# Optimization experiments

Hardware: AMD Instinct MI355X
Metric: run time of the kernel (lower is better)

## Reference

```python
import jax, jax.numpy as jnp
import numpy as np

V = 196608   # HEALPix nside=128 pixels
NNZ = 9 * V  # ~8 neighbors + self loop per pixel
B, FIN, FOUT, K = 4, 32, 64, 5


def setup_inputs() -> dict:
    key = jax.random.key(0)
    k1, k2, k3, k4, k5, k6 = jax.random.split(key, 6)
    lap_rows = jax.random.randint(k1, (NNZ,), 0, V, dtype=jnp.int32)
    lap_cols = jax.random.randint(k2, (NNZ,), 0, V, dtype=jnp.int32)
    # scale values so the Chebyshev recurrence stays numerically tame
    lap_vals = jax.random.normal(k3, (NNZ,), dtype=jnp.float32) * 0.1
    inputs = jax.random.normal(k4, (B, V, FIN), dtype=jnp.float32)
    std = np.sqrt(2.0 / (FIN + FOUT)).astype(np.float32)  # xavier normal
    weight = jax.random.normal(k5, (K, FIN, FOUT), dtype=jnp.float32) * std
    bias = jnp.full((FOUT,), 0.01, dtype=jnp.float32)
    return {"lap_rows": lap_rows, "lap_cols": lap_cols, "lap_vals": lap_vals,
            "inputs": inputs, "weight": weight, "bias": bias}


def reference(lap_rows, lap_cols, lap_vals, inputs, weight, bias):
    Bq, Vq, Fin = inputs.shape
    Kq, _, Fout = weight.shape

    # x0: [V, Fin*B]  (matches torch permute(1,2,0).reshape)
    x0 = jnp.transpose(inputs, (1, 2, 0)).reshape(Vq, Fin * Bq)

    def spmm(x):  # sparse [V,V] @ dense [V, Fin*B] via gather + scatter-add
        contrib = lap_vals[:, None] * x[lap_cols]  # [nnz, Fin*B]
        return jax.ops.segment_sum(contrib, lap_rows, num_segments=Vq)

    xs = [x0]
    if Kq > 1:
        xs.append(spmm(x0))
    for _ in range(2, Kq):
        xs.append(2.0 * spmm(xs[-1]) - xs[-2])
    cheb = jnp.stack(xs)  # [K, V, Fin*B]

    # [K,V,Fin,B] -> [B,V,Fin,K] -> [B*V, Fin*K]
    cheb = cheb.reshape(Kq, Vq, Fin, Bq).transpose(3, 1, 2, 0).reshape(Bq * Vq, Fin * Kq)
    # torch weight.view(Fin*K, Fout) flattens (K,Fin) row-major -> reshape(K*Fin, Fout)
    w2 = weight.reshape(Kq * Fin, Fout)
    out = (cheb @ w2).reshape(Bq, Vq, Fout)
    return out + bias
```

## Files before the change

### kernel.cpp

```cpp
#include <hip/hip_runtime.h>

#define V 196608
#define NNZ (9 * V)
#define B 4
#define FIN 32
#define FOUT 64
#define K 5
#define C 128
#define ROWU 64
#define SPMM_BLOCKS 2048
#define NSLICE 864
#define EDGES_PER_SLICE 2048
#define HIST_BLOCKS (NNZ / 256)
#define X0_BLOCKS (V * 16 / 256)
#define WFRAG_BLOCKS 5

typedef __attribute__((ext_vector_type(8))) short bf16x8;
typedef __attribute__((ext_vector_type(4))) float f32x4;

static __device__ __forceinline__ unsigned int f2bf(float f) {
    union { float f; unsigned int u; } v; v.f = f;
    return (v.u + 0x7FFFu + ((v.u >> 16) & 1u)) >> 16;
}
static __device__ __forceinline__ float bflo(unsigned int u) {
    union { unsigned int u; float f; } v; v.u = u << 16; return v.f;
}
static __device__ __forceinline__ float bfhi(unsigned int u) {
    union { unsigned int u; float f; } v; v.u = u & 0xFFFF0000u; return v.f;
}

__global__ void zero_cursor(uint4* __restrict__ p) {
    int t = blockIdx.x * 256 + threadIdx.x;
    if (t < V / 4) p[t] = (uint4){0u, 0u, 0u, 0u};
}

__global__ void prep_fused(const int* __restrict__ rows, int* __restrict__ cnt,
                           int* __restrict__ rank, const float* __restrict__ inp,
                           uint4* __restrict__ x0v, const float* __restrict__ w,
                           uint4* __restrict__ wfh, uint4* __restrict__ wfl) {
    const int blk = blockIdx.x;
    if (blk < HIST_BLOCKS) {
        int e = blk * 256 + threadIdx.x;
        rank[e] = atomicAdd(&cnt[rows[e]], 1);
    } else if (blk < HIST_BLOCKS + X0_BLOCKS) {
        int t = (blk - HIST_BLOCKS) * 256 + threadIdx.x;
        int v = t >> 4;
        int seg = t & 15;
        int b = seg >> 2;
        int q = seg & 3;
        const float4* s =
            reinterpret_cast<const float4*>(inp + ((size_t)b * V + v) * 32 + q * 8);
        float4 fa = s[0], fb = s[1];
        uint4 u;
        u.x = f2bf(fa.x) | (f2bf(fa.y) << 16);
        u.y = f2bf(fa.z) | (f2bf(fa.w) << 16);
        u.z = f2bf(fb.x) | (f2bf(fb.y) << 16);
        u.w = f2bf(fb.z) | (f2bf(fb.w) << 16);
        x0v[(size_t)v * 16 + seg] = u;
    } else {
        int idx = (blk - HIST_BLOCKS - X0_BLOCKS) * 256 + threadIdx.x;
        if (idx >= K * 4 * 64) return;
        int lane = idx & 63;
        int nt = (idx >> 6) & 3;
        int k = idx >> 8;
        int col = lane & 15;
        int quad = lane >> 4;
        int o = nt * 16 + col;
        unsigned int hh[8], ll[8];
#pragma unroll
        for (int e = 0; e < 8; ++e) {
            int fin = quad * 8 + e;
            float wv = w[(fin * 5 + k) * 64 + o];
            unsigned int hb = f2bf(wv);
            float hf = bflo(hb);
            ll[e] = f2bf(wv - hf);
            hh[e] = hb;
        }
        uint4 uh, ul;
        uh.x = hh[0] | (hh[1] << 16);
        uh.y = hh[2] | (hh[3] << 16);
        uh.z = hh[4] | (hh[5] << 16);
        uh.w = hh[6] | (hh[7] << 16);
        ul.x = ll[0] | (ll[1] << 16);
        ul.y = ll[2] | (ll[3] << 16);
        ul.z = ll[4] | (ll[5] << 16);
        ul.w = ll[6] | (ll[7] << 16);
        wfh[idx] = uh;
        wfl[idx] = ul;
    }
}

__global__ void chunk_sums(const int* __restrict__ cnt, int* __restrict__ bsum) {
    __shared__ int ws[16];
    int tid = threadIdx.x;
    int lane = tid & 63;
    int wid = tid >> 6;
    int v = cnt[blockIdx.x * 1024 + tid];
#pragma unroll
    for (int off = 32; off >= 1; off >>= 1) v += __shfl_down(v, off, 64);
    if (lane == 0) ws[wid] = v;
    __syncthreads();
    if (tid < 16) {
        int s = ws[tid];
#pragma unroll
        for (int off = 8; off >= 1; off >>= 1) s += __shfl_down(s, off, 16);
        if (tid == 0) bsum[blockIdx.x] = s;
    }
}

__global__ void scan_chunks2(const int* __restrict__ cnt, const int* __restrict__ bsum,
                             int* __restrict__ rowptr) {
    __shared__ int sb[192];
    __shared__ int wsum[16];
    int tid = threadIdx.x;
    int lane = tid & 63;
    int wid = tid >> 6;
    if (tid < 192) sb[tid] = bsum[tid];
    __syncthreads();
    for (int off = 1; off < 192; off <<= 1) {
        int v = (tid < 192 && tid >= off) ? sb[tid - off] : 0;
        __syncthreads();
        if (tid < 192) sb[tid] += v;
        __syncthreads();
    }
    const int bpre = (blockIdx.x == 0) ? 0 : sb[blockIdx.x - 1];
    int base = blockIdx.x * 1024;
    int v = cnt[base + tid];
    int x = v;
#pragma unroll
    for (int off = 1; off < 64; off <<= 1) {
        int t = __shfl_up(x, off, 64);
        if (lane >= off) x += t;
    }
    if (lane == 63) wsum[wid] = x;
    __syncthreads();
    if (wid == 0 && lane < 16) {
        int s = wsum[lane];
        int y = s;
#pragma unroll
        for (int off = 1; off < 16; off <<= 1) {
            int t = __shfl_up(y, off, 16);
            if (lane >= off) y += t;
        }
        wsum[lane] = y - s;
    }
    __syncthreads();
    int excl = x - v + wsum[wid] + bpre;
    rowptr[base + tid] = excl;
    if (blockIdx.x == 191 && tid == 1023) rowptr[V] = excl + v;
}

__global__ void scatter_rank(const int* __restrict__ rows, const int* __restrict__ cols,
                             const float* __restrict__ vals, const int* __restrict__ rowptr,
                             const int* __restrict__ rank, int2* __restrict__ cev) {
    const int slice = blockIdx.x >> 3;
    const int w = blockIdx.x & 7;
    const int lo = w * (NNZ / 8);
    const int hi = lo + (NNZ / 8);
    const int base = slice * EDGES_PER_SLICE;
#pragma unroll 2
    for (int i = threadIdx.x; i < EDGES_PER_SLICE; i += 256) {
        int e = base + i;
        int p = rowptr[rows[e]] + rank[e];
        if (p >= lo && p < hi) {
            int2 pk;
            pk.x = cols[e];
            pk.y = __float_as_int(vals[e]);
            cev[p] = pk;
        }
    }
}

template <int COMBINE>
__global__ __launch_bounds__(256) void spmm_gather(
    const int* __restrict__ rowptr, const int2* __restrict__ cev,
    const unsigned int* __restrict__ x, const unsigned int* __restrict__ xm2,
    unsigned int* __restrict__ y) {
    const int lane = threadIdx.x & 63;
    const int wid0 = (blockIdx.x * 256 + threadIdx.x) >> 6;
    const int NW = SPMM_BLOCKS * 4;
    for (int base = wid0 * 2; base < V; base += NW * 2) {
        const int r0 = base, r1 = base + 1;
        const int s0 = rowptr[r0];
        const int e0 = rowptr[r0 + 1];
        const int e1 = rowptr[r1 + 1];
        float ax0 = 0.f, ay0 = 0.f, ax1 = 0.f, ay1 = 0.f;
        int i0 = s0, i1 = e0;
        while (e0 - i0 >= 4 && e1 - i1 >= 4) {
            int2 Ea[4], Eb[4];
#pragma unroll
            for (int j = 0; j < 4; ++j) {
                Ea[j] = cev[i0 + j];
                Eb[j] = cev[i1 + j];
            }
            unsigned int Ua[4], Ub[4];
#pragma unroll
            for (int j = 0; j < 4; ++j) {
                Ua[j] = x[(size_t)Ea[j].x * ROWU + lane];
                Ub[j] = x[(size_t)Eb[j].x * ROWU + lane];
            }
#pragma unroll
            for (int j = 0; j < 4; ++j) {
                float va = __int_as_float(Ea[j].y);
                float vb = __int_as_float(Eb[j].y);
                ax0 = fmaf(va, bflo(Ua[j]), ax0);
                ay0 = fmaf(va, bfhi(Ua[j]), ay0);
                ax1 = fmaf(vb, bflo(Ub[j]), ax1);
                ay1 = fmaf(vb, bfhi(Ub[j]), ay1);
            }
            i0 += 4;
            i1 += 4;
        }
        while (e0 - i0 >= 4) {
            int2 Ea[4];
#pragma unroll
            for (int j = 0; j < 4; ++j) Ea[j] = cev[i0 + j];
            unsigned int Ua[4];
#pragma unroll
            for (int j = 0; j < 4; ++j) Ua[j] = x[(size_t)Ea[j].x * ROWU + lane];
#pragma unroll
            for (int j = 0; j < 4; ++j) {
                float va = __int_as_float(Ea[j].y);
                ax0 = fmaf(va, bflo(Ua[j]), ax0);
                ay0 = fmaf(va, bfhi(Ua[j]), ay0);
            }
            i0 += 4;
        }
        while (e1 - i1 >= 4) {
            int2 Eb[4];
#pragma unroll
            for (int j = 0; j < 4; ++j) Eb[j] = cev[i1 + j];
            unsigned int Ub[4];
#pragma unroll
            for (int j = 0; j < 4; ++j) Ub[j] = x[(size_t)Eb[j].x * ROWU + lane];
#pragma unroll
            for (int j = 0; j < 4; ++j) {
                float vb = __int_as_float(Eb[j].y);
                ax1 = fmaf(vb, bflo(Ub[j]), ax1);
                ay1 = fmaf(vb, bfhi(Ub[j]), ay1);
            }
            i1 += 4;
        }
        for (; i0 + 2 <= e0; i0 += 2) {
            int2 a = cev[i0], b = cev[i0 + 1];
            unsigned int u0 = x[(size_t)a.x * ROWU + lane];
            unsigned int u1 = x[(size_t)b.x * ROWU + lane];
            float v0 = __int_as_float(a.y), v1 = __int_as_float(b.y);
            ax0 = fmaf(v0, bflo(u0), ax0);
            ay0 = fmaf(v0, bfhi(u0), ay0);
            ax0 = fmaf(v1, bflo(u1), ax0);
            ay0 = fmaf(v1, bfhi(u1), ay0);
        }
        for (; i0 < e0; ++i0) {
            int2 a = cev[i0];
            unsigned int u = x[(size_t)a.x * ROWU + lane];
            float v = __int_as_float(a.y);
            ax0 = fmaf(v, bflo(u), ax0);
            ay0 = fmaf(v, bfhi(u), ay0);
        }
        for (; i1 + 2 <= e1; i1 += 2) {
            int2 a = cev[i1], b = cev[i1 + 1];
            unsigned int u0 = x[(size_t)a.x * ROWU + lane];
            unsigned int u1 = x[(size_t)b.x * ROWU + lane];
            float v0 = __int_as_float(a.y), v1 = __int_as_float(b.y);
            ax1 = fmaf(v0, bflo(u0), ax1);
            ay1 = fmaf(v0, bfhi(u0), ay1);
            ax1 = fmaf(v1, bflo(u1), ax1);
            ay1 = fmaf(v1, bfhi(u1), ay1);
        }
        for (; i1 < e1; ++i1) {
            int2 a = cev[i1];
            unsigned int u = x[(size_t)a.x * ROWU + lane];
            float v = __int_as_float(a.y);
            ax1 = fmaf(v, bflo(u), ax1);
            ay1 = fmaf(v, bfhi(u), ay1);
        }
        if (COMBINE) {
            unsigned int m0 = xm2[(size_t)r0 * ROWU + lane];
            unsigned int m1 = xm2[(size_t)r1 * ROWU + lane];
            ax0 = 2.0f * ax0 - bflo(m0);
            ay0 = 2.0f * ay0 - bfhi(m0);
            ax1 = 2.0f * ax1 - bflo(m1);
            ay1 = 2.0f * ay1 - bfhi(m1);
        }
        y[(size_t)r0 * ROWU + lane] = f2bf(ax0) | (f2bf(ay0) << 16);
        y[(size_t)r1 * ROWU + lane] = f2bf(ax1) | (f2bf(ay1) << 16);
    }
}

__global__ __launch_bounds__(256) void fused_mfma(
    const unsigned short* __restrict__ x0, const unsigned short* __restrict__ x1,
    const unsigned short* __restrict__ x2, const unsigned short* __restrict__ x3,
    const unsigned short* __restrict__ x4, const uint4* __restrict__ wfh,
    const uint4* __restrict__ wfl, const float* __restrict__ bias,
    float* __restrict__ out) {
    const int tid = threadIdx.x;
    const int lane = tid & 63;
    const int g = (blockIdx.x * 256 + tid) >> 6;
    const int v0 = g << 4;
    const int col = lane & 15;
    const int quad = lane >> 4;
    const unsigned short* const xs[K] = {x0, x1, x2, x3, x4};

    f32x4 acc[B][4];
#pragma unroll
    for (int b = 0; b < B; ++b)
#pragma unroll
        for (int nt = 0; nt < 4; ++nt) acc[b][nt] = (f32x4){0.f, 0.f, 0.f, 0.f};

#pragma unroll
    for (int k = 0; k < K; ++k) {
        const unsigned short* xk = xs[k] + ((size_t)(v0 + col)) * C + quad * 8;
        bf16x8 a0 = *reinterpret_cast<const bf16x8*>(xk);
        bf16x8 a1 = *reinterpret_cast<const bf16x8*>(xk + 32);
        bf16x8 a2 = *reinterpret_cast<const bf16x8*>(xk + 64);
        bf16x8 a3 = *reinterpret_cast<const bf16x8*>(xk + 96);
#pragma unroll
        for (int nt = 0; nt < 4; ++nt) {
            uint4 uh = wfh[(k * 4 + nt) * 64 + lane];
            uint4 ul = wfl[(k * 4 + nt) * 64 + lane];
            bf16x8 wh = *reinterpret_cast<bf16x8*>(&uh);
            bf16x8 wl = *reinterpret_cast<bf16x8*>(&ul);
            acc[0][nt] = __builtin_amdgcn_mfma_f32_16x16x32_bf16(a0, wh, acc[0][nt], 0, 0, 0);
            acc[1][nt] = __builtin_amdgcn_mfma_f32_16x16x32_bf16(a1, wh, acc[1][nt], 0, 0, 0);
            acc[2][nt] = __builtin_amdgcn_mfma_f32_16x16x32_bf16(a2, wh, acc[2][nt], 0, 0, 0);
            acc[3][nt] = __builtin_amdgcn_mfma_f32_16x16x32_bf16(a3, wh, acc[3][nt], 0, 0, 0);
            acc[0][nt] = __builtin_amdgcn_mfma_f32_16x16x32_bf16(a0, wl, acc[0][nt], 0, 0, 0);
            acc[1][nt] = __builtin_amdgcn_mfma_f32_16x16x32_bf16(a1, wl, acc[1][nt], 0, 0, 0);
            acc[2][nt] = __builtin_amdgcn_mfma_f32_16x16x32_bf16(a2, wl, acc[2][nt], 0, 0, 0);
            acc[3][nt] = __builtin_amdgcn_mfma_f32_16x16x32_bf16(a3, wl, acc[3][nt], 0, 0, 0);
        }
    }

    float bv[4];
#pragma unroll
    for (int nt = 0; nt < 4; ++nt) bv[nt] = bias[nt * 16 + col];
#pragma unroll
    for (int b = 0; b < B; ++b)
#pragma unroll
        for (int nt = 0; nt < 4; ++nt)
#pragma unroll
            for (int r = 0; r < 4; ++r) {
                int row = quad * 4 + r;
                out[((size_t)b * V + v0 + row) * FOUT + nt * 16 + col] = acc[b][nt][r] + bv[nt];
            }
}

extern "C" void kernel_launch(void* const* d_in, const int* in_sizes, int n_in,
                              void* d_out, int out_size, void* d_ws, size_t ws_size,
                              hipStream_t stream) {
    const int* lap_rows = (const int*)d_in[0];
    const int* lap_cols = (const int*)d_in[1];
    const float* lap_vals = (const float*)d_in[2];
    const float* inputs = (const float*)d_in[3];
    const float* weight = (const float*)d_in[4];
    const float* bias = (const float*)d_in[5];
    float* out = (float*)d_out;

    char* p = (char*)d_ws;
    auto alloc = [&](size_t bytes) {
        char* r = p;
        p += (bytes + 511) & ~(size_t)511;
        return r;
    };
    int* rowptr = (int*)alloc((size_t)(V + 1) * 4);
    int* cnt = (int*)alloc((size_t)V * 4);
    int* bsum = (int*)alloc(192 * 4);
    int* rank = (int*)alloc((size_t)NNZ * 4);
    uint4* wfh = (uint4*)alloc((size_t)K * 4 * 64 * 16);
    uint4* wfl = (uint4*)alloc((size_t)K * 4 * 64 * 16);
    int2* cev = (int2*)alloc((size_t)NNZ * 8);
    unsigned int* xb0 = (unsigned int*)alloc((size_t)V * ROWU * 4);
    unsigned int* xb1 = (unsigned int*)alloc((size_t)V * ROWU * 4);
    unsigned int* xb2 = (unsigned int*)alloc((size_t)V * ROWU * 4);
    unsigned int* xb3 = (unsigned int*)alloc((size_t)V * ROWU * 4);
    unsigned int* xb4 = (unsigned int*)alloc((size_t)V * ROWU * 4);

    const int mfma_blocks = (V / 16) * 64 / 256;
    const int prep_blocks = HIST_BLOCKS + X0_BLOCKS + WFRAG_BLOCKS;

    zero_cursor<<<(V / 4 + 255) / 256, 256, 0, stream>>>((uint4*)cnt);
    prep_fused<<<prep_blocks, 256, 0, stream>>>(lap_rows, cnt, rank, inputs, (uint4*)xb0,
                                                weight, wfh, wfl);
    chunk_sums<<<V / 1024, 1024, 0, stream>>>(cnt, bsum);
    scan_chunks2<<<V / 1024, 1024, 0, stream>>>(cnt, bsum, rowptr);
    scatter_rank<<<NSLICE * 8, 256, 0, stream>>>(lap_rows, lap_cols, lap_vals, rowptr,
                                                 rank, cev);

    spmm_gather<0><<<SPMM_BLOCKS, 256, 0, stream>>>(rowptr, cev, xb0, nullptr, xb1);
    spmm_gather<1><<<SPMM_BLOCKS, 256, 0, stream>>>(rowptr, cev, xb1, xb0, xb2);
    spmm_gather<1><<<SPMM_BLOCKS, 256, 0, stream>>>(rowptr, cev, xb2, xb1, xb3);
    spmm_gather<1><<<SPMM_BLOCKS, 256, 0, stream>>>(rowptr, cev, xb3, xb2, xb4);

    fused_mfma<<<mfma_blocks, 256, 0, stream>>>(
        (const unsigned short*)xb0, (const unsigned short*)xb1, (const unsigned short*)xb2,
        (const unsigned short*)xb3, (const unsigned short*)xb4, wfh, wfl, bias, out);
}
```

Baseline: 623.6 us.

## Privatize row histogram into eight copies and simplify CSR scatter to one pass

```diff
diff --git a/kernel.cpp b/kernel.cpp
--- a/kernel.cpp
+++ b/kernel.cpp
@@ -9,8 +9,6 @@
 #define C 128
 #define ROWU 64
 #define SPMM_BLOCKS 2048
-#define NSLICE 864
-#define EDGES_PER_SLICE 2048
 #define HIST_BLOCKS (NNZ / 256)
 #define X0_BLOCKS (V * 16 / 256)
 #define WFRAG_BLOCKS 5
@@ -29,19 +27,20 @@
     union { unsigned int u; float f; } v; v.u = u & 0xFFFF0000u; return v.f;
 }
 
-__global__ void zero_cursor(uint4* __restrict__ p) {
+__global__ void zero_cnt8(uint4* __restrict__ p) {
     int t = blockIdx.x * 256 + threadIdx.x;
-    if (t < V / 4) p[t] = (uint4){0u, 0u, 0u, 0u};
-}
-
-__global__ void prep_fused(const int* __restrict__ rows, int* __restrict__ cnt,
+    if (t < 2 * V) p[t] = (uint4){0u, 0u, 0u, 0u};
+}
+
+__global__ void prep_fused(const int* __restrict__ rows, int* __restrict__ cnt8,
                            int* __restrict__ rank, const float* __restrict__ inp,
                            uint4* __restrict__ x0v, const float* __restrict__ w,
                            uint4* __restrict__ wfh, uint4* __restrict__ wfl) {
     const int blk = blockIdx.x;
     if (blk < HIST_BLOCKS) {
         int e = blk * 256 + threadIdx.x;
-        rank[e] = atomicAdd(&cnt[rows[e]], 1);
+        int c = blk & 7;
+        rank[e] = atomicAdd(&cnt8[c * V + rows[e]], 1);
     } else if (blk < HIST_BLOCKS + X0_BLOCKS) {
         int t = (blk - HIST_BLOCKS) * 256 + threadIdx.x;
         int v = t >> 4;
@@ -90,12 +89,15 @@
     }
 }
 
-__global__ void chunk_sums(const int* __restrict__ cnt, int* __restrict__ bsum) {
+__global__ void chunk_sums(const int* __restrict__ cnt8, int* __restrict__ bsum) {
     __shared__ int ws[16];
     int tid = threadIdx.x;
     int lane = tid & 63;
     int wid = tid >> 6;
-    int v = cnt[blockIdx.x * 1024 + tid];
+    int r = blockIdx.x * 1024 + tid;
+    int v = 0;
+#pragma unroll
+    for (int x = 0; x < 8; ++x) v += cnt8[x * V + r];
 #pragma unroll
     for (int off = 32; off >= 1; off >>= 1) v += __shfl_down(v, off, 64);
     if (lane == 0) ws[wid] = v;
@@ -108,8 +110,8 @@
     }
 }
 
-__global__ void scan_chunks2(const int* __restrict__ cnt, const int* __restrict__ bsum,
-                             int* __restrict__ rowptr) {
+__global__ void scan_chunks2(const int* __restrict__ cnt8, const int* __restrict__ bsum,
+                             int* __restrict__ rowptr, int* __restrict__ off8) {
     __shared__ int sb[192];
     __shared__ int wsum[16];
     int tid = threadIdx.x;
@@ -124,8 +126,15 @@
         __syncthreads();
     }
     const int bpre = (blockIdx.x == 0) ? 0 : sb[blockIdx.x - 1];
-    int base = blockIdx.x * 1024;
-    int v = cnt[base + tid];
+    int r = blockIdx.x * 1024 + tid;
+    int tot = 0;
+#pragma unroll
+    for (int x = 0; x < 8; ++x) {
+        int cv = cnt8[x * V + r];
+        off8[x * V + r] = tot;
+        tot += cv;
+    }
+    int v = tot;
     int x = v;
 #pragma unroll
     for (int off = 1; off < 64; off <<= 1) {
@@ -146,29 +155,22 @@
     }
     __syncthreads();
     int excl = x - v + wsum[wid] + bpre;
-    rowptr[base + tid] = excl;
+    rowptr[r] = excl;
     if (blockIdx.x == 191 && tid == 1023) rowptr[V] = excl + v;
 }
 
 __global__ void scatter_rank(const int* __restrict__ rows, const int* __restrict__ cols,
                              const float* __restrict__ vals, const int* __restrict__ rowptr,
-                             const int* __restrict__ rank, int2* __restrict__ cev) {
-    const int slice = blockIdx.x >> 3;
-    const int w = blockIdx.x & 7;
-    const int lo = w * (NNZ / 8);
-    const int hi = lo + (NNZ / 8);
-    const int base = slice * EDGES_PER_SLICE;
-#pragma unroll 2
-    for (int i = threadIdx.x; i < EDGES_PER_SLICE; i += 256) {
-        int e = base + i;
-        int p = rowptr[rows[e]] + rank[e];
-        if (p >= lo && p < hi) {
-            int2 pk;
-            pk.x = cols[e];
-            pk.y = __float_as_int(vals[e]);
-            cev[p] = pk;
-        }
-    }
+                             const int* __restrict__ rank, const int* __restrict__ off8,
+                             int2* __restrict__ cev) {
+    int e = blockIdx.x * 256 + threadIdx.x;
+    int r = rows[e];
+    int c = (e >> 8) & 7;
+    int p = rowptr[r] + off8[c * V + r] + rank[e];
+    int2 pk;
+    pk.x = cols[e];
+    pk.y = __float_as_int(vals[e]);
+    cev[p] = pk;
 }
 
 template <int COMBINE>
@@ -364,7 +366,8 @@
         return r;
     };
     int* rowptr = (int*)alloc((size_t)(V + 1) * 4);
-    int* cnt = (int*)alloc((size_t)V * 4);
+    int* cnt8 = (int*)alloc((size_t)8 * V * 4);
+    int* off8 = (int*)alloc((size_t)8 * V * 4);
     int* bsum = (int*)alloc(192 * 4);
     int* rank = (int*)alloc((size_t)NNZ * 4);
     uint4* wfh = (uint4*)alloc((size_t)K * 4 * 64 * 16);
@@ -378,14 +381,15 @@
 
     const int mfma_blocks = (V / 16) * 64 / 256;
     const int prep_blocks = HIST_BLOCKS + X0_BLOCKS + WFRAG_BLOCKS;
-
-    zero_cursor<<<(V / 4 + 255) / 256, 256, 0, stream>>>((uint4*)cnt);
-    prep_fused<<<prep_blocks, 256, 0, stream>>>(lap_rows, cnt, rank, inputs, (uint4*)xb0,
+    const int edge_blocks = NNZ / 256;
+
+    zero_cnt8<<<(2 * V + 255) / 256, 256, 0, stream>>>((uint4*)cnt8);
+    prep_fused<<<prep_blocks, 256, 0, stream>>>(lap_rows, cnt8, rank, inputs, (uint4*)xb0,
                                                 weight, wfh, wfl);
-    chunk_sums<<<V / 1024, 1024, 0, stream>>>(cnt, bsum);
-    scan_chunks2<<<V / 1024, 1024, 0, stream>>>(cnt, bsum, rowptr);
-    scatter_rank<<<NSLICE * 8, 256, 0, stream>>>(lap_rows, lap_cols, lap_vals, rowptr,
-                                                 rank, cev);
+    chunk_sums<<<V / 1024, 1024, 0, stream>>>(cnt8, bsum);
+    scan_chunks2<<<V / 1024, 1024, 0, stream>>>(cnt8, bsum, rowptr, off8);
+    scatter_rank<<<edge_blocks, 256, 0, stream>>>(lap_rows, lap_cols, lap_vals, rowptr,
+                                                  rank, off8, cev);
 
     spmm_gather<0><<<SPMM_BLOCKS, 256, 0, stream>>>(rowptr, cev, xb0, nullptr, xb1);
     spmm_gather<1><<<SPMM_BLOCKS, 256, 0, stream>>>(rowptr, cev, xb1, xb0, xb2);
```

Result: faster. 587.2 us (-5.8%).
